# Kernel tuning notes

Hardware: AMD Instinct MI355X
Metric: run time of the kernel (lower is better)

## Reference

```python
import jax, jax.numpy as jnp
import numpy as np

TAU_MIN, TAU_MAX = 5.0, 50.0
BOOST = 3.2
DECO_RATE = 0.01

B, I, F, Q = 4096, 1024, 2048, 4

def setup_inputs() -> dict:
    key = jax.random.key(0)
    ks = jax.random.split(key, 12)
    return {
        "inputs": jax.random.normal(ks[0], (B, I), jnp.float32),
        "hidden_state": jax.random.normal(ks[1], (B, F), jnp.float32),
        "W_in": jax.random.normal(ks[2], (I, F), jnp.float32) / np.sqrt(I),
        "b_in": jnp.zeros((F,), jnp.float32),
        "amp_real": jax.random.normal(ks[3], (F, Q), jnp.float32) * 0.1,
        "amp_imag": jax.random.normal(ks[4], (F, Q), jnp.float32) * 0.1,
        "phase": jax.random.uniform(ks[5], (F, Q), jnp.float32, 0.0, 2 * np.pi),
        "primary": jax.random.normal(ks[6], (F, F), jnp.float32) / np.sqrt(F),
        "ent_mat": jax.random.normal(ks[7], (F, F), jnp.float32) / np.sqrt(F),
        "corr": jax.random.uniform(ks[8], (F,), jnp.float32, 0.0, 0.7),
        "W_tau": jax.random.uniform(ks[9], (F, F), jnp.float32, 0.0, 0.1) / np.sqrt(F),
        "b_tau": jnp.zeros((F,), jnp.float32),
        "W_dec": jax.random.uniform(ks[10], (F, F), jnp.float32, 0.0, 0.5) / np.sqrt(F),
        "b_dec": jnp.zeros((F,), jnp.float32),
        "time_step": 1,
    }

def reference(inputs, hidden_state, W_in, b_in, amp_real, amp_imag, phase,
              primary, ent_mat, corr, W_tau, b_tau, W_dec, b_dec, time_step):
    t = jnp.float32(time_step)
    batch = inputs.shape[0]
    feats = hidden_state.shape[1]

    # input projection: [B,I] @ [I,F]
    x_proj = inputs @ W_in + b_in

    # quantum superposition state (batch-independent, [F,Q] params)
    ph = phase + t * 0.1
    real_c = amp_real * jnp.cos(ph)          # [F,Q]
    imag_c = amp_imag * jnp.sin(ph)          # [F,Q]
    sup_r = real_c.sum(-1)                    # [F]
    sup_i = imag_c.sum(-1)                    # [F]
    prob_amp = real_c ** 2 + imag_c ** 2      # [F,Q]
    q_state = sup_r * jnp.exp(-sup_i ** 2)    # [F]
    q_state_b = jnp.broadcast_to(q_state, (batch, feats))
    prob_amp_b = jnp.broadcast_to(prob_amp, (batch,) + prob_amp.shape)

    # entangled recurrent connections: two F x F matmuls
    ent_rec = hidden_state @ primary + (hidden_state @ ent_mat) * corr

    # quantum time constants
    tau_raw = q_state_b @ W_tau + b_tau
    tau_q = (TAU_MIN + (TAU_MAX - TAU_MIN) * jax.nn.sigmoid(tau_raw)) / BOOST

    # decoherence gate
    deco = jax.nn.sigmoid(q_state_b @ W_dec + b_dec)
    coherent = jnp.exp(-DECO_RATE * t)

    classical = jnp.tanh(x_proj + ent_rec)
    quantum_act = q_state_b * deco * coherent
    combined = classical + quantum_act

    dx_dt = (-hidden_state + combined) / tau_q
    dt_q = 0.1 / BOOST
    new_hidden = hidden_state + dt_q * dx_dt

    # diagnostics
    d_amp = jnp.mean(prob_amp_b, axis=-1)          # [B,F]
    d_coh = coherent
    d_ent = jnp.mean(jnp.abs(ent_rec))
    d_dec = jnp.mean(deco)
    d_tau = jnp.mean(tau_q)
    return (new_hidden, d_amp, d_coh, d_ent, d_dec, d_tau)
```

## Files before the change

kernel.cpp:

```cpp
#include <hip/hip_runtime.h>
#include <hip/hip_bf16.h>

#define BD 4096
#define ID 1024
#define FD 2048

typedef __bf16 v8bf __attribute__((ext_vector_type(8)));
typedef float  v4f  __attribute__((ext_vector_type(4)));

struct alignas(8) bf4 { __hip_bfloat16 x, y, z, w; };

__device__ inline __hip_bfloat16 bf(float f) { return __float2bfloat16(f); }
__device__ inline float sig(float x) { return 1.f / (1.f + expf(-x)); }

__device__ inline void gload16(const __hip_bfloat16* g, __hip_bfloat16* l) {
  __builtin_amdgcn_global_load_lds(
      (const __attribute__((address_space(1))) void*)g,
      (__attribute__((address_space(3))) void*)l, 16, 0, 0);
}

__global__ void k_prep_q(const float* ar, const float* ai, const float* ph,
                         const int* tstep, float* qs, float* pamp,
                         float* scal, float* tau_raw, float* dec_raw) {
  int j = blockIdx.x * 256 + threadIdx.x;
  if (j < 4) scal[j] = 0.f;
  if (j < FD) { tau_raw[j] = 0.f; dec_raw[j] = 0.f; }
  if (j >= FD) return;
  float t = (float)tstep[0];
  float4 a = ((const float4*)ar)[j];
  float4 b = ((const float4*)ai)[j];
  float4 p = ((const float4*)ph)[j];
  float sr = 0.f, si = 0.f, pm = 0.f;
  {
    float c, s, rc, ic;
    c = cosf(p.x + 0.1f * t); s = sinf(p.x + 0.1f * t);
    rc = a.x * c; ic = b.x * s; sr += rc; si += ic; pm += rc * rc + ic * ic;
    c = cosf(p.y + 0.1f * t); s = sinf(p.y + 0.1f * t);
    rc = a.y * c; ic = b.y * s; sr += rc; si += ic; pm += rc * rc + ic * ic;
    c = cosf(p.z + 0.1f * t); s = sinf(p.z + 0.1f * t);
    rc = a.z * c; ic = b.z * s; sr += rc; si += ic; pm += rc * rc + ic * ic;
    c = cosf(p.w + 0.1f * t); s = sinf(p.w + 0.1f * t);
    rc = a.w * c; ic = b.w * s; sr += rc; si += ic; pm += rc * rc + ic * ic;
  }
  qs[j] = sr * expf(-si * si);
  pamp[j] = 0.25f * pm;
}

__global__ void k_cast(const float* s1, __hip_bfloat16* d1, int n1,
                       const float* s2, __hip_bfloat16* d2) {
  int i = blockIdx.x * blockDim.x + threadIdx.x;
  const float* src = s1; __hip_bfloat16* dst = d1;
  if (i >= n1) { i -= n1; src = s2; dst = d2; }
  float4 v = ((const float4*)src)[i];
  bf4 o{bf(v.x), bf(v.y), bf(v.z), bf(v.w)};
  ((bf4*)dst)[i] = o;
}

__global__ void k_tcast(const float* src, const float* src2, const float* corr,
                        __hip_bfloat16* dst, int R, int C, int useM) {
  __shared__ float t[32][33];
  int tx = threadIdx.x, ty = threadIdx.y;
  int x = blockIdx.x * 32 + tx;
  int yb = blockIdx.y * 32;
  float cr = useM ? corr[x] : 0.f;
#pragma unroll
  for (int j = 0; j < 4; j++) {
    int y = yb + ty + j * 8;
    float v = src[(size_t)y * C + x];
    if (useM) v += src2[(size_t)y * C + x] * cr;
    t[ty + j * 8][tx] = v;
  }
  __syncthreads();
#pragma unroll
  for (int j = 0; j < 4; j++) {
    int orow = blockIdx.x * 32 + ty + j * 8;
    int ocol = yb + tx;
    dst[(size_t)orow * R + ocol] = bf(t[tx][ty + j * 8]);
  }
}

__global__ void k_matvec(const float* qs, const float* Wt, const float* Wd,
                         float* tau_raw, float* dec_raw) {
  int j = blockIdx.x * 256 + threadIdx.x;
  int i0 = blockIdx.y * 128;
  const float* W = blockIdx.z ? Wd : Wt;
  float* out = blockIdx.z ? dec_raw : tau_raw;
  __shared__ float q[128];
  if (threadIdx.x < 128) q[threadIdx.x] = qs[i0 + threadIdx.x];
  __syncthreads();
  float acc = 0.f;
#pragma unroll 8
  for (int i = 0; i < 128; i++) acc = fmaf(q[i], W[(size_t)(i0 + i) * FD + j], acc);
  atomicAdd(&out[j], acc);
}

__global__ void k_post(const float* tau_raw, const float* dec_raw, const float* qs,
                       const float* b_tau, const float* b_dec, const int* tstep,
                       float* s_arr, float* qact, float* scal) {
  int j = blockIdx.x * 256 + threadIdx.x;
  float t = (float)tstep[0];
  float coh = expf(-0.01f * t);
  float tq = (5.f + 45.f * sig(tau_raw[j] + b_tau[j])) / 3.2f;
  s_arr[j] = 0.03125f / tq;
  float dec = sig(dec_raw[j] + b_dec[j]);
  qact[j] = qs[j] * dec * coh;
  float tsum = tq, dsum = dec;
  for (int off = 32; off; off >>= 1) {
    tsum += __shfl_down(tsum, off);
    dsum += __shfl_down(dsum, off);
  }
  __shared__ float rt[4], rd[4];
  int w = threadIdx.x >> 6;
  if ((threadIdx.x & 63) == 0) { rt[w] = tsum; rd[w] = dsum; }
  __syncthreads();
  if (threadIdx.x == 0) {
    atomicAdd(&scal[1], rd[0] + rd[1] + rd[2] + rd[3]);
    atomicAdd(&scal[2], rt[0] + rt[1] + rt[2] + rt[3]);
  }
}

__global__ __launch_bounds__(256, 4) void k_gemm(
    const __hip_bfloat16* __restrict__ Ah,
    const __hip_bfloat16* __restrict__ MT,
    const __hip_bfloat16* __restrict__ Ax,
    const __hip_bfloat16* __restrict__ WT,
    const float* __restrict__ b_in, const float* __restrict__ s_arr,
    const float* __restrict__ qact,
    float* ent_sum, float* __restrict__ out) {
  __shared__ alignas(16) __hip_bfloat16 As[2][128][32];
  __shared__ alignas(16) __hip_bfloat16 Bs[2][64][32];
  __shared__ float red[4];

  const int tid = threadIdx.x;
  const int l = tid & 63, w = tid >> 6;
  const int wr = w >> 1, wc = w & 1;
  const int row0 = blockIdx.x * 128, col0 = blockIdx.y * 64;

  v4f acc[4][2];
#pragma unroll
  for (int i = 0; i < 4; i++)
#pragma unroll
    for (int j = 0; j < 2; j++) acc[i][j] = (v4f)0.f;

  const int srow = l >> 2;
  const int scol = ((l & 3) ^ ((l >> 3) & 3)) * 8;
  const int rcol = ((l >> 4) ^ ((l >> 1) & 3)) * 8;

  auto stage = [&](int buf, const __hip_bfloat16* A, int lda,
                   const __hip_bfloat16* B, int ldb, int k) {
    gload16(A + (size_t)(row0 + w * 32 + srow) * lda + k + scol,
            &As[buf][w * 32][0]);
    gload16(A + (size_t)(row0 + w * 32 + 16 + srow) * lda + k + scol,
            &As[buf][w * 32 + 16][0]);
    gload16(B + (size_t)(col0 + w * 16 + srow) * ldb + k + scol,
            &Bs[buf][w * 16][0]);
  };
  auto compute = [&](int buf) {
    v8bf a[4], b[2];
#pragma unroll
    for (int mi = 0; mi < 4; mi++)
      a[mi] = *(const v8bf*)&As[buf][wr * 64 + mi * 16 + (l & 15)][rcol];
#pragma unroll
    for (int ni = 0; ni < 2; ni++)
      b[ni] = *(const v8bf*)&Bs[buf][wc * 32 + ni * 16 + (l & 15)][rcol];
#pragma unroll
    for (int mi = 0; mi < 4; mi++)
#pragma unroll
      for (int ni = 0; ni < 2; ni++)
        acc[mi][ni] = __builtin_amdgcn_mfma_f32_16x16x32_bf16(a[mi], b[ni], acc[mi][ni], 0, 0, 0);
  };

  stage(0, Ah, FD, MT, FD, 0);
  __syncthreads();
  for (int kt = 0; kt < FD / 32; kt++) {
    if (kt + 1 < FD / 32) stage((kt + 1) & 1, Ah, FD, MT, FD, (kt + 1) * 32);
    compute(kt & 1);
    __syncthreads();
  }

  float asum = 0.f;
#pragma unroll
  for (int mi = 0; mi < 4; mi++)
#pragma unroll
    for (int ni = 0; ni < 2; ni++)
#pragma unroll
      for (int e = 0; e < 4; e++) asum += fabsf(acc[mi][ni][e]);

  stage(0, Ax, ID, WT, ID, 0);
  __syncthreads();
  for (int kt = 0; kt < ID / 32; kt++) {
    if (kt + 1 < ID / 32) stage((kt + 1) & 1, Ax, ID, WT, ID, (kt + 1) * 32);
    compute(kt & 1);
    __syncthreads();
  }

  for (int off = 32; off; off >>= 1) asum += __shfl_down(asum, off);
  if (l == 0) red[w] = asum;
  __syncthreads();
  if (tid == 0) atomicAdd(ent_sum, red[0] + red[1] + red[2] + red[3]);

#pragma unroll
  for (int ni = 0; ni < 2; ni++) {
    int gc = col0 + wc * 32 + ni * 16 + (l & 15);
    float bi = b_in[gc], qa = qact[gc], sj = s_arr[gc];
#pragma unroll
    for (int mi = 0; mi < 4; mi++) {
      int gr0 = row0 + wr * 64 + mi * 16 + (l >> 4) * 4;
#pragma unroll
      for (int e = 0; e < 4; e++) {
        int gr = gr0 + e;
        float comb = tanhf(acc[mi][ni][e] + bi) + qa;
        float h = __bfloat162float(Ah[(size_t)gr * FD + gc]);
        out[(size_t)gr * FD + gc] = fmaf(sj, comb - h, h);
      }
    }
  }
}

__global__ void k_damp(const float* __restrict__ pamp, const float* scal,
                       const int* tstep, float* __restrict__ out1, float* out3) {
  int i = blockIdx.x * 256 + threadIdx.x;
  int c = (i * 4) & (FD - 1);
  ((float4*)out1)[i] = *(const float4*)&pamp[c];
  if (i == 0) {
    float t = (float)tstep[0];
    out3[0] = expf(-0.01f * t);
    out3[1] = scal[0] / (float)((size_t)BD * FD);
    out3[2] = scal[1] / (float)FD;
    out3[3] = scal[2] / (float)FD;
  }
}

extern "C" void kernel_launch(void* const* d_in, const int* in_sizes, int n_in,
                              void* d_out, int out_size, void* d_ws, size_t ws_size,
                              hipStream_t stream) {
  const float* inputs  = (const float*)d_in[0];
  const float* hidden  = (const float*)d_in[1];
  const float* W_in    = (const float*)d_in[2];
  const float* b_in    = (const float*)d_in[3];
  const float* amp_r   = (const float*)d_in[4];
  const float* amp_i   = (const float*)d_in[5];
  const float* phase   = (const float*)d_in[6];
  const float* primary = (const float*)d_in[7];
  const float* ent_mat = (const float*)d_in[8];
  const float* corr    = (const float*)d_in[9];
  const float* W_tau   = (const float*)d_in[10];
  const float* b_tau   = (const float*)d_in[11];
  const float* W_dec   = (const float*)d_in[12];
  const float* b_dec   = (const float*)d_in[13];
  const int*   tstep   = (const int*)d_in[14];

  char* ws = (char*)d_ws;
  __hip_bfloat16* inputs_bf = (__hip_bfloat16*)(ws + 0);
  __hip_bfloat16* hidden_bf = (__hip_bfloat16*)(ws + 8388608);
  __hip_bfloat16* WT        = (__hip_bfloat16*)(ws + 25165824);
  __hip_bfloat16* MT        = (__hip_bfloat16*)(ws + 29360128);
  char* sb = ws + 37748736;
  float* scal    = (float*)(sb);
  float* qs      = (float*)(sb + 16);
  float* pamp    = (float*)(sb + 16 + 8192);
  float* tau_raw = (float*)(sb + 16 + 2 * 8192);
  float* dec_raw = (float*)(sb + 16 + 3 * 8192);
  float* s_arr   = (float*)(sb + 16 + 4 * 8192);
  float* qact    = (float*)(sb + 16 + 5 * 8192);

  float* out = (float*)d_out;

  hipLaunchKernelGGL(k_prep_q, dim3(8), dim3(256), 0, stream,
                     amp_r, amp_i, phase, tstep, qs, pamp, scal, tau_raw, dec_raw);
  hipLaunchKernelGGL(k_cast, dim3(12288), dim3(256), 0, stream,
                     inputs, inputs_bf, BD * ID / 4, hidden, hidden_bf);
  hipLaunchKernelGGL(k_tcast, dim3(64, 32), dim3(32, 8), 0, stream,
                     W_in, (const float*)nullptr, (const float*)nullptr, WT, ID, FD, 0);
  hipLaunchKernelGGL(k_tcast, dim3(64, 64), dim3(32, 8), 0, stream,
                     primary, ent_mat, corr, MT, FD, FD, 1);
  hipLaunchKernelGGL(k_matvec, dim3(8, 16, 2), dim3(256), 0, stream, qs, W_tau, W_dec, tau_raw, dec_raw);
  hipLaunchKernelGGL(k_post, dim3(8), dim3(256), 0, stream, tau_raw, dec_raw, qs, b_tau, b_dec, tstep, s_arr, qact, scal);
  hipLaunchKernelGGL(k_gemm, dim3(32, 32), dim3(256), 0, stream,
                     hidden_bf, MT, inputs_bf, WT, b_in, s_arr, qact,
                     &scal[0], out);
  hipLaunchKernelGGL(k_damp, dim3(8192), dim3(256), 0, stream,
                     pamp, scal, tstep, out + (size_t)BD * FD, out + (size_t)2 * BD * FD);
}
```

Measured before the change: 142.7 us.

## Triple-buffer the GEMM with a unified pipeline across both K phases

Merges the hidden-state GEMM loop and the input-projection GEMM loop into one 96-step loop. The loop uses three LDS buffers and prefetches two stages ahead. Each step waits only on the oldest outstanding global_load_lds group (vmcnt(3)) and then issues a raw s_barrier, replacing the per-iteration __syncthreads and the pipeline drain and refill between the two GEMMs. This should overlap memory latency with MFMA work more fully, at the cost of 50% more LDS per block, which could limit occupancy, and a fragile hand-written waitcnt/barrier schedule.

Result: no change. 143.2 us (+0.4%).

```diff
diff --git a/kernel.cpp b/kernel.cpp
--- a/kernel.cpp
+++ b/kernel.cpp
@@ -4,6 +4,7 @@
 #define BD 4096
 #define ID 1024
 #define FD 2048
+#define NT 96
 
 typedef __bf16 v8bf __attribute__((ext_vector_type(8)));
 typedef float  v4f  __attribute__((ext_vector_type(4)));
@@ -127,8 +128,8 @@
     const float* __restrict__ b_in, const float* __restrict__ s_arr,
     const float* __restrict__ qact,
     float* ent_sum, float* __restrict__ out) {
-  __shared__ alignas(16) __hip_bfloat16 As[2][128][32];
-  __shared__ alignas(16) __hip_bfloat16 Bs[2][64][32];
+  __shared__ alignas(16) __hip_bfloat16 As[3][128][32];
+  __shared__ alignas(16) __hip_bfloat16 Bs[3][64][32];
   __shared__ float red[4];
 
   const int tid = threadIdx.x;
@@ -146,16 +147,21 @@
   const int scol = ((l & 3) ^ ((l >> 3) & 3)) * 8;
   const int rcol = ((l >> 4) ^ ((l >> 1) & 3)) * 8;
 
-  auto stage = [&](int buf, const __hip_bfloat16* A, int lda,
-                   const __hip_bfloat16* B, int ldb, int k) {
-    gload16(A + (size_t)(row0 + w * 32 + srow) * lda + k + scol,
+  auto stage = [&](int t) {
+    int buf = t % 3;
+    const __hip_bfloat16* A = (t < 64) ? Ah : Ax;
+    const __hip_bfloat16* B = (t < 64) ? MT : WT;
+    int ld = (t < 64) ? FD : ID;
+    int k = (t & 63) * 32;
+    gload16(A + (size_t)(row0 + w * 32 + srow) * ld + k + scol,
             &As[buf][w * 32][0]);
-    gload16(A + (size_t)(row0 + w * 32 + 16 + srow) * lda + k + scol,
+    gload16(A + (size_t)(row0 + w * 32 + 16 + srow) * ld + k + scol,
             &As[buf][w * 32 + 16][0]);
-    gload16(B + (size_t)(col0 + w * 16 + srow) * ldb + k + scol,
+    gload16(B + (size_t)(col0 + w * 16 + srow) * ld + k + scol,
             &Bs[buf][w * 16][0]);
   };
-  auto compute = [&](int buf) {
+  auto compute = [&](int t) {
+    int buf = t % 3;
     v8bf a[4], b[2];
 #pragma unroll
     for (int mi = 0; mi < 4; mi++)
@@ -170,29 +176,31 @@
         acc[mi][ni] = __builtin_amdgcn_mfma_f32_16x16x32_bf16(a[mi], b[ni], acc[mi][ni], 0, 0, 0);
   };
 
-  stage(0, Ah, FD, MT, FD, 0);
-  __syncthreads();
-  for (int kt = 0; kt < FD / 32; kt++) {
-    if (kt + 1 < FD / 32) stage((kt + 1) & 1, Ah, FD, MT, FD, (kt + 1) * 32);
-    compute(kt & 1);
-    __syncthreads();
-  }
+  stage(0);
+  __builtin_amdgcn_sched_barrier(0);
+  stage(1);
 
   float asum = 0.f;
-#pragma unroll
-  for (int mi = 0; mi < 4; mi++)
-#pragma unroll
-    for (int ni = 0; ni < 2; ni++)
-#pragma unroll
-      for (int e = 0; e < 4; e++) asum += fabsf(acc[mi][ni][e]);
-
-  stage(0, Ax, ID, WT, ID, 0);
-  __syncthreads();
-  for (int kt = 0; kt < ID / 32; kt++) {
-    if (kt + 1 < ID / 32) stage((kt + 1) & 1, Ax, ID, WT, ID, (kt + 1) * 32);
-    compute(kt & 1);
-    __syncthreads();
-  }
+
+  for (int t = 0; t < NT - 1; t++) {
+    asm volatile("s_waitcnt vmcnt(3)" ::: "memory");
+    __builtin_amdgcn_s_barrier();
+    __builtin_amdgcn_sched_barrier(0);
+    if (t + 2 < NT) stage(t + 2);
+    compute(t);
+    if (t == 63) {
+#pragma unroll
+      for (int mi = 0; mi < 4; mi++)
+#pragma unroll
+        for (int ni = 0; ni < 2; ni++)
+#pragma unroll
+          for (int e = 0; e < 4; e++) asum += fabsf(acc[mi][ni][e]);
+    }
+  }
+  asm volatile("s_waitcnt vmcnt(0)" ::: "memory");
+  __builtin_amdgcn_s_barrier();
+  __builtin_amdgcn_sched_barrier(0);
+  compute(NT - 1);
 
   for (int off = 32; off; off >>= 1) asum += __shfl_down(asum, off);
   if (l == 0) red[w] = asum;
```
